# Performance work log

Measured on AMD Instinct MI355X. Metric: run time of the kernel, lower is better.

Reference implementation:

```python
import jax, jax.numpy as jnp
import numpy as np
from itertools import combinations

NUM_ENT = 7
DIM_ENT = 256
REL_HIDDEN = 256
HIDDEN = 1024
BATCH = 16384
PAIRS = np.array(list(combinations(range(NUM_ENT), 2)), dtype=np.int32)  # [21, 2]


def setup_inputs() -> dict:
    key = jax.random.key(0)
    k1, k2, k3 = jax.random.split(key, 3)
    ctx = jax.random.normal(k1, (BATCH, NUM_ENT * DIM_ENT), dtype=jnp.float32)
    # torch init: uniform(-init_range, init_range) weights, zero bias
    W_rel = jax.random.uniform(k2, (2 * DIM_ENT, REL_HIDDEN), dtype=jnp.float32, minval=-0.01, maxval=0.01)
    b_rel = jnp.zeros((REL_HIDDEN,), dtype=jnp.float32)
    W_fc = jax.random.uniform(k3, (NUM_ENT * DIM_ENT + REL_HIDDEN, HIDDEN), dtype=jnp.float32, minval=-0.01, maxval=0.01)
    b_fc = jnp.zeros((HIDDEN,), dtype=jnp.float32)
    return {"ctx": ctx, "W_rel": W_rel, "b_rel": b_rel, "W_fc": W_fc, "b_fc": b_fc}


def reference(ctx, W_rel, b_rel, W_fc, b_fc):
    B = ctx.shape[0]
    ents = ctx.reshape(B, NUM_ENT, DIM_ENT)
    idx_i = jnp.asarray(PAIRS[:, 0])
    idx_j = jnp.asarray(PAIRS[:, 1])
    # gather both endpoints of each of the 21 pairs: [B, 21, 2*DIM_ENT]
    pair_feat = jnp.concatenate([ents[:, idx_i, :], ents[:, idx_j, :]], axis=-1)
    # batched small Linear + Tanh: [B, 21, REL_HIDDEN]
    rel = jnp.tanh(jnp.einsum("bpe,eh->bph", pair_feat, W_rel) + b_rel)
    # faithful replication of torch: cat pair-major then view(B, rel_hidden, -1).sum(2)
    rel = rel.reshape(B, 21 * REL_HIDDEN).reshape(B, REL_HIDDEN, 21).sum(axis=2)
    inpt = jnp.concatenate([ctx, rel], axis=1)  # [B, input_size]
    # dropout output is discarded in the original forward (no-op); fc1 uses inpt
    out = jnp.tanh(inpt @ W_fc + b_fc)
    return out[None, :, :]  # [1, B, HIDDEN]
```

## Files before the change

### kernel.cpp

```cpp
#include <hip/hip_runtime.h>

typedef unsigned short u16;
typedef unsigned int u32;
typedef __attribute__((ext_vector_type(8))) short short8;
typedef __attribute__((ext_vector_type(4))) float f32x4;
typedef const __attribute__((address_space(1))) unsigned int g_u32;
typedef __attribute__((address_space(3))) unsigned int l_u32;

#define BATCH 16384
#define XCOLS 2048

__device__ __forceinline__ void gload16(const void* g, void* l) {
  __builtin_amdgcn_global_load_lds((g_u32*)g, (l_u32*)l, 16, 0, 0);
}
__device__ __forceinline__ u16 f2bf(float f) {
  u32 x = __builtin_bit_cast(u32, f);
  x += 0x7fffu + ((x >> 16) & 1u);
  return (u16)(x >> 16);
}
__device__ __forceinline__ int swz(int P) { return P ^ (((P >> 7) & 7) << 4); }

__device__ __forceinline__ float fast_tanh(float x) {
  float e = __builtin_amdgcn_exp2f(x * 2.885390081777927f);
  return __builtin_fmaf(-2.0f, __builtin_amdgcn_rcpf(e + 1.0f), 1.0f);
}

#define PIPK 0544333222211111000000ULL
#define PJPK 0665654654365432654321ULL

__global__ void prep_ctx(const float* __restrict__ ctx, u16* __restrict__ X) {
  const int total = BATCH * 224;
  for (int u = blockIdx.x * blockDim.x + threadIdx.x; u < total;
       u += gridDim.x * blockDim.x) {
    int b = u / 224, c8 = u - b * 224;
    const float4* s = (const float4*)(ctx + (size_t)b * 1792 + c8 * 8);
    float4 v0 = s[0], v1 = s[1];
    short8 o;
    o[0] = (short)f2bf(v0.x); o[1] = (short)f2bf(v0.y);
    o[2] = (short)f2bf(v0.z); o[3] = (short)f2bf(v0.w);
    o[4] = (short)f2bf(v1.x); o[5] = (short)f2bf(v1.y);
    o[6] = (short)f2bf(v1.z); o[7] = (short)f2bf(v1.w);
    *(short8*)(X + (size_t)b * XCOLS + c8 * 8) = o;
  }
}

__global__ void prep_wrel(const float* __restrict__ Wr, u16* __restrict__ WcT) {
  int idx = blockIdx.x * 256 + threadIdx.x;
  if (idx >= 512 * 256) return;
  int n = idx >> 8, k = idx & 255;
  float v = (n < 256) ? Wr[k * 256 + n] : Wr[(256 + k) * 256 + (n - 256)];
  WcT[idx] = f2bf(v);
}

__global__ void prep_wfc(const float* __restrict__ W, u16* __restrict__ WT) {
  __shared__ float t[64][65];
  int k0 = blockIdx.x * 64;
  int n0 = blockIdx.y * 64;
  int tx = threadIdx.x & 63, ty = threadIdx.x >> 6;
  #pragma unroll
  for (int i = 0; i < 64; i += 4)
    t[ty + i][tx] = W[(size_t)(k0 + ty + i) * 1024 + n0 + tx];
  __syncthreads();
  #pragma unroll
  for (int i = 0; i < 64; i += 4) {
    int n = ty + i;
    WT[(size_t)(n0 + n) * XCOLS + k0 + tx] = f2bf(t[tx][n]);
  }
}

__global__ __launch_bounds__(512, 4) void gemm1_fused(u16* __restrict__ X, const u16* __restrict__ WcT,
                                                      const float* __restrict__ b_rel) {
  __shared__ __align__(16) u16 smem[36864];
  char* sb = (char*)smem;
  const int tid = threadIdx.x;
  const int wid = tid >> 6, lane = tid & 63;
  const int b_base = blockIdx.x * 8;
  f32x4 bias[4] = {};
  if (wid < 4) {
    #pragma unroll
    for (int n = 0; n < 4; ++n)
      bias[n] = *(const f32x4*)(b_rel + wid * 64 + n * 16 + ((lane >> 4) << 2));
  }
  f32x4 acc[4][4] = {};
  for (int kt = 0; kt < 4; ++kt) {
    const int kb = kt * 64;
    {
      int L = swz(tid * 16);
      int row = L >> 7, koff = (L & 127) >> 1;
      int r = row < 56 ? row : 55;
      int bl = r / 7, e = r - bl * 7;
      gload16(X + (size_t)(b_base + bl) * XCOLS + e * 256 + kb + koff, sb + wid * 1024);
    }
    #pragma unroll
    for (int i = 0; i < 8; ++i) {
      int slot = i * 512 + tid;
      int L = swz(slot * 16);
      int rn = L >> 7, koff = (L & 127) >> 1;
      gload16(WcT + rn * 256 + kb + koff, sb + 8192 + (i * 512 + wid * 64) * 16);
    }
    __syncthreads();
    #pragma unroll
    for (int kk = 0; kk < 64; kk += 32) {
      short8 a[4], b[4];
      #pragma unroll
      for (int m = 0; m < 4; ++m) {
        int row = m * 16 + (lane & 15);
        int L = row * 128 + kk * 2 + ((lane >> 4) << 4);
        a[m] = *(const short8*)(sb + swz(L));
      }
      #pragma unroll
      for (int n = 0; n < 4; ++n) {
        int rn = wid * 64 + n * 16 + (lane & 15);
        int L = rn * 128 + kk * 2 + ((lane >> 4) << 4);
        b[n] = *(const short8*)(sb + 8192 + swz(L));
      }
      #pragma unroll
      for (int m = 0; m < 4; ++m)
        #pragma unroll
        for (int n = 0; n < 4; ++n)
          acc[m][n] = __builtin_amdgcn_mfma_f32_16x16x32_bf16(b[n], a[m], acc[m][n], 0, 0, 0);
    }
    __syncthreads();
  }
  auto stage = [&](int rd) {
    #pragma unroll
    for (int m = 0; m < 4; ++m) {
      int row = m * 16 + (lane & 15);
      int lr = row - rd * 14;
      if (lr >= 0 && lr < 14) {
        #pragma unroll
        for (int n = 0; n < 4; ++n) {
          f32x4 val = acc[m][n] + bias[n];
          int h0c = wid * 64 + n * 16 + ((lane >> 4) << 2);
          int L = lr * 2048 + h0c * 4;
          *(f32x4*)(sb + (L ^ ((lr & 7) << 4))) = val;
        }
      }
    }
  };
  stage(0);
  const int bb = tid >> 8;
  const int r = tid & 255;
  const int R21 = r * 21;
  const int p0 = R21 >> 8;
  const int h0 = R21 & 255;
  const int cx = 256 - h0;
  const int p1 = p0 < 20 ? p0 + 1 : 20;
  const int li0 = bb * 7 + (int)((PIPK >> (3 * p0)) & 7);
  const int lj0 = bb * 7 + (int)((PJPK >> (3 * p0)) & 7);
  const int li1 = bb * 7 + (int)((PIPK >> (3 * p1)) & 7);
  const int lj1 = bb * 7 + (int)((PJPK >> (3 * p1)) & 7);
  const int bU0 = li0 * 2048 + h0 * 4, sU0 = (li0 & 7) << 4;
  const int bV0 = lj0 * 2048 + 1024 + h0 * 4, sV0 = (lj0 & 7) << 4;
  const int bU1 = li1 * 2048 - cx * 4, sU1 = (li1 & 7) << 4;
  const int bV1 = lj1 * 2048 + 1024 - cx * 4, sV1 = (lj1 & 7) << 4;
  __syncthreads();
  for (int rd = 0; rd < 4; ++rd) {
    float s = 0.f;
    #pragma unroll
    for (int c = 0; c < 21; ++c) {
      bool sg = c >= cx;
      int aU = ((sg ? bU1 : bU0) + 4 * c) ^ (sg ? sU1 : sU0);
      int aV = ((sg ? bV1 : bV0) + 4 * c) ^ (sg ? sV1 : sV0);
      float u = *(const float*)(sb + aU);
      float v = *(const float*)(sb + aV);
      s += fast_tanh(u + v);
    }
    X[(size_t)(b_base + rd * 2 + bb) * XCOLS + 1792 + r] = f2bf(s);
    __syncthreads();
    if (rd < 3) {
      stage(rd + 1);
      __syncthreads();
    }
  }
}

#define G2_BUF 49152
__global__ __launch_bounds__(512, 2) void gemm2(const u16* __restrict__ X, const u16* __restrict__ WT,
                                                const float* __restrict__ b_fc, float* __restrict__ out) {
  __shared__ __align__(16) u16 smem[73728];
  char* sb = (char*)smem;
  const int tid = threadIdx.x;
  const int wid = tid >> 6, lane = tid & 63;
  const int wr = wid >> 2, wc = wid & 3;
  int bid = blockIdx.x;
  int sw = (bid & 7) * 64 + (bid >> 3);
  int bm = sw >> 3, bn = sw & 7;
  const size_t mBase = (size_t)bm * 256;
  const int nBase = bn * 128;
  f32x4 acc[8][2] = {};
  auto stage2 = [&](int t, int q) {
    char* Ab = sb + q * G2_BUF;
    char* Bb = Ab + 32768;
    const int kb = t * 64;
    #pragma unroll
    for (int i = 0; i < 4; ++i) {
      int L = swz((i * 512 + tid) * 16);
      int row = L >> 7, koff = (L & 127) >> 1;
      gload16(X + (mBase + row) * XCOLS + kb + koff, Ab + (i * 512 + wid * 64) * 16);
    }
    #pragma unroll
    for (int i = 0; i < 2; ++i) {
      int L = swz((i * 512 + tid) * 16);
      int row = L >> 7, koff = (L & 127) >> 1;
      gload16(WT + (size_t)(nBase + row) * XCOLS + kb + koff, Bb + (i * 512 + wid * 64) * 16);
    }
  };
  auto compute = [&](int q) {
    char* Ab = sb + q * G2_BUF;
    char* Bb = Ab + 32768;
    #pragma unroll
    for (int kk = 0; kk < 64; kk += 32) {
      short8 a[8], b[2];
      #pragma unroll
      for (int m = 0; m < 8; ++m) {
        int row = wr * 128 + m * 16 + (lane & 15);
        int L = row * 128 + kk * 2 + ((lane >> 4) << 4);
        a[m] = *(const short8*)(Ab + swz(L));
      }
      #pragma unroll
      for (int n = 0; n < 2; ++n) {
        int rn = wc * 32 + n * 16 + (lane & 15);
        int L = rn * 128 + kk * 2 + ((lane >> 4) << 4);
        b[n] = *(const short8*)(Bb + swz(L));
      }
      __builtin_amdgcn_s_setprio(1);
      #pragma unroll
      for (int m = 0; m < 8; ++m)
        #pragma unroll
        for (int n = 0; n < 2; ++n)
          acc[m][n] = __builtin_amdgcn_mfma_f32_16x16x32_bf16(a[m], b[n], acc[m][n], 0, 0, 0);
      __builtin_amdgcn_s_setprio(0);
    }
  };
  stage2(0, 0);
  stage2(1, 1);
  int qc = 0;
  for (int t = 0; t < 31; ++t) {
    asm volatile("s_waitcnt vmcnt(6)" ::: "memory");
    __builtin_amdgcn_s_barrier();
    if (t < 30) {
      int qs = qc + 2 >= 3 ? qc - 1 : qc + 2;
      stage2(t + 2, qs);
    }
    compute(qc);
    qc = qc + 1 >= 3 ? 0 : qc + 1;
  }
  asm volatile("s_waitcnt vmcnt(0)" ::: "memory");
  __builtin_amdgcn_s_barrier();
  compute(qc);
  #pragma unroll
  for (int m = 0; m < 8; ++m) {
    int row0 = wr * 128 + m * 16 + ((lane >> 4) << 2);
    #pragma unroll
    for (int n = 0; n < 2; ++n) {
      int col = nBase + wc * 32 + n * 16 + (lane & 15);
      float bias = b_fc[col];
      #pragma unroll
      for (int v = 0; v < 4; ++v)
        out[(mBase + row0 + v) * 1024 + col] = fast_tanh(acc[m][n][v] + bias);
    }
  }
}

extern "C" void kernel_launch(void* const* d_in, const int* in_sizes, int n_in,
                              void* d_out, int out_size, void* d_ws, size_t ws_size,
                              hipStream_t stream) {
  const float* ctx   = (const float*)d_in[0];
  const float* W_rel = (const float*)d_in[1];
  const float* b_rel = (const float*)d_in[2];
  const float* W_fc  = (const float*)d_in[3];
  const float* b_fc  = (const float*)d_in[4];
  float* out = (float*)d_out;
  u16* X    = (u16*)d_ws;
  u16* WcT  = X + (size_t)BATCH * XCOLS;
  u16* WfcT = WcT + 512 * 256;
  prep_ctx<<<2048, 256, 0, stream>>>(ctx, X);
  prep_wrel<<<512, 256, 0, stream>>>(W_rel, WcT);
  prep_wfc<<<dim3(32, 16), 256, 0, stream>>>(W_fc, WfcT);
  gemm1_fused<<<2048, 512, 0, stream>>>(X, WcT, b_rel);
  gemm2<<<512, 512, 0, stream>>>(X, WfcT, b_fc, out);
}
```

Baseline: 206.7 us.

## Fuse ctx bf16 conversion into gemm1 and double-buffer the pair-sum staging

Removes the separate prep_ctx kernel. gemm1 now reads fp32 ctx directly, converts it to bf16 in registers, writes it to LDS for the MFMA and to the X workspace for gemm2. This avoids one full read and write pass over the bf16 copy of ctx plus a kernel launch. The U/V staging buffer for the tanh pair-sum is now double-buffered with a padded row stride instead of an XOR swizzle, which drops one barrier per round. In exchange, the ctx loads are now synchronous register loads rather than async global-to-LDS loads, and the padded layout may bring back LDS bank conflicts.

```diff
diff --git a/kernel.cpp b/kernel.cpp
--- a/kernel.cpp
+++ b/kernel.cpp
@@ -9,6 +9,8 @@
 
 #define BATCH 16384
 #define XCOLS 2048
+#define UVROW 2064
+#define UVBUF 28896
 
 __device__ __forceinline__ void gload16(const void* g, void* l) {
   __builtin_amdgcn_global_load_lds((g_u32*)g, (l_u32*)l, 16, 0, 0);
@@ -27,22 +29,6 @@
 
 #define PIPK 0544333222211111000000ULL
 #define PJPK 0665654654365432654321ULL
-
-__global__ void prep_ctx(const float* __restrict__ ctx, u16* __restrict__ X) {
-  const int total = BATCH * 224;
-  for (int u = blockIdx.x * blockDim.x + threadIdx.x; u < total;
-       u += gridDim.x * blockDim.x) {
-    int b = u / 224, c8 = u - b * 224;
-    const float4* s = (const float4*)(ctx + (size_t)b * 1792 + c8 * 8);
-    float4 v0 = s[0], v1 = s[1];
-    short8 o;
-    o[0] = (short)f2bf(v0.x); o[1] = (short)f2bf(v0.y);
-    o[2] = (short)f2bf(v0.z); o[3] = (short)f2bf(v0.w);
-    o[4] = (short)f2bf(v1.x); o[5] = (short)f2bf(v1.y);
-    o[6] = (short)f2bf(v1.z); o[7] = (short)f2bf(v1.w);
-    *(short8*)(X + (size_t)b * XCOLS + c8 * 8) = o;
-  }
-}
 
 __global__ void prep_wrel(const float* __restrict__ Wr, u16* __restrict__ WcT) {
   int idx = blockIdx.x * 256 + threadIdx.x;
@@ -68,7 +54,9 @@
   }
 }
 
-__global__ __launch_bounds__(512, 4) void gemm1_fused(u16* __restrict__ X, const u16* __restrict__ WcT,
+__global__ __launch_bounds__(512, 4) void gemm1_fused(const float* __restrict__ ctx,
+                                                      u16* __restrict__ X,
+                                                      const u16* __restrict__ WcT,
                                                       const float* __restrict__ b_rel) {
   __shared__ __align__(16) u16 smem[36864];
   char* sb = (char*)smem;
@@ -81,16 +69,18 @@
     for (int n = 0; n < 4; ++n)
       bias[n] = *(const f32x4*)(b_rel + wid * 64 + n * 16 + ((lane >> 4) << 2));
   }
+  const int La = swz(tid * 16);
+  const int arow = La >> 7;
+  const int akoff = (La & 127) >> 1;
+  const int arc = arow < 56 ? arow : 55;
+  const int abl = arc / 7, ae = arc - abl * 7;
+  const float* asrc = ctx + (size_t)(b_base + abl) * 1792 + ae * 256 + akoff;
+  u16* xdst = X + (size_t)(b_base + abl) * XCOLS + ae * 256 + akoff;
   f32x4 acc[4][4] = {};
   for (int kt = 0; kt < 4; ++kt) {
     const int kb = kt * 64;
-    {
-      int L = swz(tid * 16);
-      int row = L >> 7, koff = (L & 127) >> 1;
-      int r = row < 56 ? row : 55;
-      int bl = r / 7, e = r - bl * 7;
-      gload16(X + (size_t)(b_base + bl) * XCOLS + e * 256 + kb + koff, sb + wid * 1024);
-    }
+    float4 a0 = *(const float4*)(asrc + kb);
+    float4 a1 = *(const float4*)(asrc + kb + 4);
     #pragma unroll
     for (int i = 0; i < 8; ++i) {
       int slot = i * 512 + tid;
@@ -98,6 +88,13 @@
       int rn = L >> 7, koff = (L & 127) >> 1;
       gload16(WcT + rn * 256 + kb + koff, sb + 8192 + (i * 512 + wid * 64) * 16);
     }
+    short8 o;
+    o[0] = (short)f2bf(a0.x); o[1] = (short)f2bf(a0.y);
+    o[2] = (short)f2bf(a0.z); o[3] = (short)f2bf(a0.w);
+    o[4] = (short)f2bf(a1.x); o[5] = (short)f2bf(a1.y);
+    o[6] = (short)f2bf(a1.z); o[7] = (short)f2bf(a1.w);
+    *(short8*)(sb + tid * 16) = o;
+    if (arow < 56) *(short8*)(xdst + kb) = o;
     __syncthreads();
     #pragma unroll
     for (int kk = 0; kk < 64; kk += 32) {
@@ -123,6 +120,7 @@
     __syncthreads();
   }
   auto stage = [&](int rd) {
+    char* ub = sb + (rd & 1) * UVBUF;
     #pragma unroll
     for (int m = 0; m < 4; ++m) {
       int row = m * 16 + (lane & 15);
@@ -132,8 +130,7 @@
         for (int n = 0; n < 4; ++n) {
           f32x4 val = acc[m][n] + bias[n];
           int h0c = wid * 64 + n * 16 + ((lane >> 4) << 2);
-          int L = lr * 2048 + h0c * 4;
-          *(f32x4*)(sb + (L ^ ((lr & 7) << 4))) = val;
+          *(f32x4*)(ub + lr * UVROW + h0c * 4) = val;
         }
       }
     }
@@ -150,28 +147,24 @@
   const int lj0 = bb * 7 + (int)((PJPK >> (3 * p0)) & 7);
   const int li1 = bb * 7 + (int)((PIPK >> (3 * p1)) & 7);
   const int lj1 = bb * 7 + (int)((PJPK >> (3 * p1)) & 7);
-  const int bU0 = li0 * 2048 + h0 * 4, sU0 = (li0 & 7) << 4;
-  const int bV0 = lj0 * 2048 + 1024 + h0 * 4, sV0 = (lj0 & 7) << 4;
-  const int bU1 = li1 * 2048 - cx * 4, sU1 = (li1 & 7) << 4;
-  const int bV1 = lj1 * 2048 + 1024 - cx * 4, sV1 = (lj1 & 7) << 4;
+  const int bU0 = li0 * UVROW + h0 * 4;
+  const int bV0 = lj0 * UVROW + 1024 + h0 * 4;
+  const int bU1 = li1 * UVROW - cx * 4;
+  const int bV1 = lj1 * UVROW + 1024 - cx * 4;
   __syncthreads();
   for (int rd = 0; rd < 4; ++rd) {
+    const char* ub = sb + (rd & 1) * UVBUF;
     float s = 0.f;
     #pragma unroll
     for (int c = 0; c < 21; ++c) {
       bool sg = c >= cx;
-      int aU = ((sg ? bU1 : bU0) + 4 * c) ^ (sg ? sU1 : sU0);
-      int aV = ((sg ? bV1 : bV0) + 4 * c) ^ (sg ? sV1 : sV0);
-      float u = *(const float*)(sb + aU);
-      float v = *(const float*)(sb + aV);
+      float u = *(const float*)(ub + (sg ? bU1 : bU0) + 4 * c);
+      float v = *(const float*)(ub + (sg ? bV1 : bV0) + 4 * c);
       s += fast_tanh(u + v);
     }
     X[(size_t)(b_base + rd * 2 + bb) * XCOLS + 1792 + r] = f2bf(s);
+    if (rd < 3) stage(rd + 1);
     __syncthreads();
-    if (rd < 3) {
-      stage(rd + 1);
-      __syncthreads();
-    }
   }
 }
 
@@ -275,9 +268,8 @@
   u16* X    = (u16*)d_ws;
   u16* WcT  = X + (size_t)BATCH * XCOLS;
   u16* WfcT = WcT + 512 * 256;
-  prep_ctx<<<2048, 256, 0, stream>>>(ctx, X);
   prep_wrel<<<512, 256, 0, stream>>>(W_rel, WcT);
   prep_wfc<<<dim3(32, 16), 256, 0, stream>>>(W_fc, WfcT);
-  gemm1_fused<<<2048, 512, 0, stream>>>(X, WcT, b_rel);
+  gemm1_fused<<<2048, 512, 0, stream>>>(ctx, X, WcT, b_rel);
   gemm2<<<512, 512, 0, stream>>>(X, WfcT, b_fc, out);
 }
```

New measurement: 291.8 us. 41.2% more time.
